# Optimization experiments

Hardware: AMD Instinct MI355X
Metric: run time of the kernel (lower is better)

Reference implementation:

```python
import jax, jax.numpy as jnp
import numpy as np

B, T = 64, 4096
K = 67            # 25 body + 21 + 21 hand keypoints
D = 256           # first_layer_size
C = 7             # num_classes
THR = 0.1         # confidence_threshold
EPS = 1e-5        # BatchNorm eps


def setup_inputs() -> dict:
    key = jax.random.key(0)
    ks = jax.random.split(key, 8)
    body = jax.random.normal(ks[0], (B, T, 75), dtype=jnp.float32)
    hand_right = jax.random.normal(ks[1], (B, T, 63), dtype=jnp.float32)
    hand_left = jax.random.normal(ks[2], (B, T, 63), dtype=jnp.float32)
    length = jax.random.randint(ks[3], (B,), 1, T + 1, dtype=jnp.int64)
    W1 = jax.random.normal(ks[4], (2 * K, D), dtype=jnp.float32) * 0.05
    b1 = jnp.zeros((D,), dtype=jnp.float32)
    gamma = jnp.ones((D,), dtype=jnp.float32)
    beta = jnp.zeros((D,), dtype=jnp.float32)
    Wc = jax.random.normal(ks[5], (D, C), dtype=jnp.float32) * 0.05
    bc = jnp.zeros((C,), dtype=jnp.float32)
    return {"body": body, "hand_right": hand_right, "hand_left": hand_left,
            "length": length, "W1": W1, "b1": b1, "gamma": gamma,
            "beta": beta, "Wc": Wc, "bc": bc}


def reference(body, hand_right, hand_left, length, W1, b1, gamma, beta, Wc, bc):
    # concat keypoint streams -> [B, T, 3K] -> [B, T, K, 3]
    feats = jnp.concatenate([body, hand_right, hand_left], axis=2)
    feats = feats.reshape(feats.shape[0], feats.shape[1], -1, 3)
    x, y, conf = feats[..., 0], feats[..., 1], feats[..., 2]
    conf = (conf > THR).astype(feats.dtype)
    # gate coords by confidence, flatten to [B, T, 2K]
    pos = jnp.stack([x * conf, y * conf], axis=3)
    pos = pos.reshape(pos.shape[0], pos.shape[1], -1)
    # static MLP: Linear + ReLU -> [B, T, D]
    sf = jax.nn.relu(jnp.einsum("btf,fd->btd", pos, W1) + b1)
    # masked max pool over valid timesteps (vectorized segment-max)
    mask = jnp.arange(sf.shape[1])[None, :] < length[:, None]      # [B, T]
    pooled = jnp.max(jnp.where(mask[:, :, None], sf, -jnp.inf), axis=1)  # [B, D]
    # BatchNorm1d (training mode: batch statistics)
    mean = pooled.mean(axis=0)
    var = pooled.var(axis=0)
    bn = (pooled - mean) / jnp.sqrt(var + EPS) * gamma + beta
    # classifier
    return bn @ Wc + bc
```

## Files before the change

### kernel.cpp

```cpp
#include <hip/hip_runtime.h>
#include <hip/hip_bf16.h>

#define B_   64
#define T_   4096
#define K_   67
#define F_   134
#define FP_  160
#define D_   256
#define C_   7
#define THR_ 0.1f
#define EPS_ 1e-5f
#define NXB_ 16

typedef __bf16 bf16x8 __attribute__((ext_vector_type(8)));
typedef float  f32x4  __attribute__((ext_vector_type(4)));

typedef __attribute__((address_space(1))) const unsigned int guint;
typedef __attribute__((address_space(3))) unsigned int luint;


__device__ __forceinline__ int get_len(const int* L, int b) {
    return (L[1] == 0) ? L[2 * b] : L[b];
}

__global__ void convert_w1(const float* __restrict__ W1, __bf16* __restrict__ W1bf) {
    __shared__ float tile[32][33];
    const int d0 = blockIdx.x * 32, f0 = blockIdx.y * 32;
    const int tx = threadIdx.x & 31, ty = threadIdx.x >> 5;
#pragma unroll
    for (int r = 0; r < 32; r += 8) {
        int f = f0 + ty + r;
        tile[ty + r][tx] = (f < F_) ? W1[f * D_ + d0 + tx] : 0.f;
    }
    __syncthreads();
#pragma unroll
    for (int r = 0; r < 32; r += 8) {
        int d = d0 + ty + r;
        W1bf[d * FP_ + f0 + tx] = (__bf16)tile[tx][ty + r];
    }
}

__global__ __launch_bounds__(256, 2)
void fused_mlp_pool(const float* __restrict__ body,
                    const float* __restrict__ hr,
                    const float* __restrict__ hl,
                    const int*   __restrict__ length,
                    const float* __restrict__ b1,
                    const __bf16* __restrict__ W1bf,
                    float* __restrict__ pooled)
{
    const int b   = blockIdx.y;
    const int len = get_len(length, b);
    const int nt  = (len + 31) >> 5;
    if ((int)blockIdx.x >= nt) return;

    __shared__ __align__(16) float  raw[2][6432];
    __shared__ __align__(16) __bf16 As[10 * 512];

    const int tid  = threadIdx.x;
    const int wave = tid >> 6;
    const int lane = tid & 63;
    const int quad = lane >> 4;
    const int l16  = lane & 15;
    const int dbase = wave * 64;

    const long rowb = (long)b * T_;

    auto stage = [&](int jt, int bufi) {
        const float* bodyt = body + (rowb + (long)jt * 32) * 75;
        const float* hrt   = hr   + (rowb + (long)jt * 32) * 63;
        const float* hlt   = hl   + (rowb + (long)jt * 32) * 63;
        char* rw = (char*)raw[bufi];
        for (int i = wave; i < 10; i += 4) {
            int off = i * 256 + lane * 4;
            if (off < 2400)
                __builtin_amdgcn_global_load_lds((guint*)(bodyt + off),
                                                 (luint*)(rw + off * 4), 16, 0, 0);
        }
        for (int i = wave; i < 8; i += 4) {
            int off = i * 256 + lane * 4;
            if (off < 2016) {
                __builtin_amdgcn_global_load_lds((guint*)(hrt + off),
                                                 (luint*)(rw + 9600 + off * 4), 16, 0, 0);
                __builtin_amdgcn_global_load_lds((guint*)(hlt + off),
                                                 (luint*)(rw + 17664 + off * 4), 16, 0, 0);
            }
        }
    };

    stage(blockIdx.x, 0);

    bf16x8 bfrag[4][5];
    float  b1v[4];
#pragma unroll
    for (int n = 0; n < 4; n++) {
        int d = dbase + n * 16 + l16;
        const __bf16* p = W1bf + d * FP_ + quad * 8;
#pragma unroll
        for (int kt = 0; kt < 5; kt++)
            bfrag[n][kt] = *(const bf16x8*)(p + kt * 32);
        b1v[n] = b1[d];
    }

    int roffv[8], wv[8];
    {
        const int t  = ((tid >> 5) & 3) * 8 + ((tid >> 2) & 7);
        const int kb = ((tid >> 7) & 1) * 4 + (tid & 3);
#pragma unroll
        for (int it = 0; it < 8; it++) {
            int k = it * 8 + kb;
            roffv[it] = (k < 25) ? t * 75 + 3 * k
                       : (k < 46) ? 2400 + t * 63 + 3 * (k - 25)
                                  : 4416 + t * 63 + 3 * (k - 46);
            wv[it] = ((t >> 4) * 5 + (k >> 4)) * 256
                   + (((k >> 2) & 3) * 16 + (t & 15)) * 4 + (k & 3);
        }
    }
    int roff_c = 0, w_c = 0;
    if (tid < 96) {
        int t = tid & 31, k = 64 + (tid >> 5);
        roff_c = 4416 + t * 63 + 3 * (k - 46);
        w_c = ((t >> 4) * 5 + (k >> 4)) * 256
            + (((k >> 2) & 3) * 16 + (t & 15)) * 4 + (k & 3);
    }

    for (int i = tid; i < 416; i += 256) {
        int t = i & 31, kp = 67 + (i >> 5);
        int w = ((t >> 4) * 5 + (kp >> 4)) * 256
              + (((kp >> 2) & 3) * 16 + (t & 15)) * 4 + (kp & 3);
        ((unsigned int*)As)[w] = 0u;
    }

    float runmax[4] = {0.f, 0.f, 0.f, 0.f};
    int cur = 0;

    for (int j = blockIdx.x; j < nt; j += NXB_) {
        const bool hasnext = (j + NXB_ < nt);
        if (hasnext) stage(j + NXB_, cur ^ 1);

        if (hasnext) {
            if (wave < 2) asm volatile("s_waitcnt vmcnt(7) lgkmcnt(0)\n\ts_barrier" ::: "memory");
            else          asm volatile("s_waitcnt vmcnt(6) lgkmcnt(0)\n\ts_barrier" ::: "memory");
        } else {
            asm volatile("s_waitcnt vmcnt(0) lgkmcnt(0)\n\ts_barrier" ::: "memory");
        }

        const float* rw = raw[cur];
#pragma unroll
        for (int it = 0; it < 8; it++) {
            float x = rw[roffv[it]], y = rw[roffv[it] + 1], cf = rw[roffv[it] + 2];
            bool g = cf > THR_;
            x = g ? x : 0.f;  y = g ? y : 0.f;
            unsigned short ux = __builtin_bit_cast(unsigned short, (__bf16)x);
            unsigned short uy = __builtin_bit_cast(unsigned short, (__bf16)y);
            ((unsigned int*)As)[wv[it]] = (unsigned int)ux | ((unsigned int)uy << 16);
        }
        if (tid < 96) {
            float x = rw[roff_c], y = rw[roff_c + 1], cf = rw[roff_c + 2];
            bool g = cf > THR_;
            x = g ? x : 0.f;  y = g ? y : 0.f;
            unsigned short ux = __builtin_bit_cast(unsigned short, (__bf16)x);
            unsigned short uy = __builtin_bit_cast(unsigned short, (__bf16)y);
            ((unsigned int*)As)[w_c] = (unsigned int)ux | ((unsigned int)uy << 16);
        }

        asm volatile("s_waitcnt lgkmcnt(0)\n\ts_barrier" ::: "memory");

        f32x4 acc[2][4];
#pragma unroll
        for (int m = 0; m < 2; m++)
#pragma unroll
            for (int n = 0; n < 4; n++)
                acc[m][n] = (f32x4){0.f, 0.f, 0.f, 0.f};
#pragma unroll
        for (int kt = 0; kt < 5; kt++) {
#pragma unroll
            for (int m = 0; m < 2; m++) {
                bf16x8 a = *(const bf16x8*)(As + (m * 5 + kt) * 512 + lane * 8);
#pragma unroll
                for (int n = 0; n < 4; n++)
                    acc[m][n] = __builtin_amdgcn_mfma_f32_16x16x32_bf16(a, bfrag[n][kt], acc[m][n], 0, 0, 0);
            }
        }

        const int tt0 = j * 32;
#pragma unroll
        for (int m = 0; m < 2; m++) {
            int trow0 = tt0 + m * 16 + quad * 4;
#pragma unroll
            for (int r = 0; r < 4; r++) {
                bool valid = (trow0 + r) < len;
#pragma unroll
                for (int n = 0; n < 4; n++) {
                    float v = acc[m][n][r] + b1v[n];
                    v = (v > 0.f) ? v : 0.f;
                    runmax[n] = (valid && v > runmax[n]) ? v : runmax[n];
                }
            }
        }
        cur ^= 1;
    }

#pragma unroll
    for (int n = 0; n < 4; n++) {
        float r = runmax[n];
        r = fmaxf(r, __shfl_xor(r, 16, 64));
        r = fmaxf(r, __shfl_xor(r, 32, 64));
        if (quad == n) {
            atomicMax((unsigned int*)(pooled + b * D_ + dbase + n * 16 + l16),
                      __float_as_uint(r));
        }
    }
}

__global__ void bn_classifier(const float* __restrict__ pooled,
                              const float* __restrict__ gamma,
                              const float* __restrict__ beta,
                              const float* __restrict__ Wc,
                              const float* __restrict__ bc,
                              float* __restrict__ out)
{
    __shared__ float scale_s[D_], shift_s[D_];
    const int tid = threadIdx.x;
    float s = 0.f, ss = 0.f;
#pragma unroll 8
    for (int b = 0; b < B_; b++) {
        float v = pooled[b * D_ + tid];
        s += v; ss += v * v;
    }
    float mean = s * (1.f / B_);
    float var  = ss * (1.f / B_) - mean * mean;
    var = fmaxf(var, 0.f);
    float sc = gamma[tid] * rsqrtf(var + EPS_);
    scale_s[tid] = sc;
    shift_s[tid] = beta[tid] - mean * sc;

    const int wv = tid >> 6, ln = tid & 63;
    float wcr[4][C_];
#pragma unroll
    for (int j = 0; j < 4; j++)
#pragma unroll
        for (int c = 0; c < C_; c++)
            wcr[j][c] = Wc[(ln * 4 + j) * C_ + c];
    __syncthreads();

    for (int b = wv * 16; b < wv * 16 + 16; b++) {
        float4 v = *(const float4*)(pooled + b * D_ + ln * 4);
        float q[4];
        q[0] = v.x * scale_s[ln * 4 + 0] + shift_s[ln * 4 + 0];
        q[1] = v.y * scale_s[ln * 4 + 1] + shift_s[ln * 4 + 1];
        q[2] = v.z * scale_s[ln * 4 + 2] + shift_s[ln * 4 + 2];
        q[3] = v.w * scale_s[ln * 4 + 3] + shift_s[ln * 4 + 3];
        float p[C_];
#pragma unroll
        for (int c = 0; c < C_; c++) p[c] = 0.f;
#pragma unroll
        for (int j = 0; j < 4; j++)
#pragma unroll
            for (int c = 0; c < C_; c++)
                p[c] += q[j] * wcr[j][c];
#pragma unroll
        for (int c = 0; c < C_; c++) {
#pragma unroll
            for (int off = 1; off < 64; off <<= 1)
                p[c] += __shfl_xor(p[c], off, 64);
        }
        if (ln == 0) {
#pragma unroll
            for (int c = 0; c < C_; c++)
                out[b * C_ + c] = p[c] + bc[c];
        }
    }
}

extern "C" void kernel_launch(void* const* d_in, const int* in_sizes, int n_in,
                              void* d_out, int out_size, void* d_ws, size_t ws_size,
                              hipStream_t stream) {
    const float* body   = (const float*)d_in[0];
    const float* hr     = (const float*)d_in[1];
    const float* hl     = (const float*)d_in[2];
    const int*   length = (const int*)  d_in[3];
    const float* W1     = (const float*)d_in[4];
    const float* b1     = (const float*)d_in[5];
    const float* gamma  = (const float*)d_in[6];
    const float* beta   = (const float*)d_in[7];
    const float* Wc     = (const float*)d_in[8];
    const float* bc     = (const float*)d_in[9];
    float* out = (float*)d_out;

    float*  pooled = (float*)d_ws;
    __bf16* W1bf   = (__bf16*)((char*)d_ws + 65536);

    hipMemsetAsync(d_ws, 0, 65536, stream);
    convert_w1<<<dim3(8, 5), dim3(256), 0, stream>>>(W1, W1bf);
    fused_mlp_pool<<<dim3(NXB_, B_), dim3(256), 0, stream>>>(body, hr, hl, length, b1, W1bf, pooled);
    bn_classifier<<<dim3(1), dim3(256), 0, stream>>>(pooled, gamma, beta, Wc, bc, out);
}
```

Before: 229.4 us.

## Rebalance pooling tiles across batches and deepen load/repack/MFMA pipeline

Uses a 1D grid in which each block handles up to eight 32-step tiles taken from eight rotated batch rows. Before, each block owned a single batch row, so work per block followed that row's length; the new mapping spreads valid tiles more evenly across blocks. The kernel also double-buffers the bf16 A tile, so the repack of the next tile overlaps the MFMAs of the current one, and it stages two tiles ahead. MFMA issue priority is raised during the matmul. In exchange it issues one atomicMax per tile instead of one per block, uses more LDS, and adds bitmask bookkeeping to skip empty tiles.

```diff
diff --git a/kernel.cpp b/kernel.cpp
--- a/kernel.cpp
+++ b/kernel.cpp
@@ -3,14 +3,13 @@
 
 #define B_   64
 #define T_   4096
-#define K_   67
 #define F_   134
 #define FP_  160
 #define D_   256
 #define C_   7
 #define THR_ 0.1f
 #define EPS_ 1e-5f
-#define NXB_ 16
+#define NQ_  16
 
 typedef __bf16 bf16x8 __attribute__((ext_vector_type(8)));
 typedef float  f32x4  __attribute__((ext_vector_type(4)));
@@ -18,10 +17,9 @@
 typedef __attribute__((address_space(1))) const unsigned int guint;
 typedef __attribute__((address_space(3))) unsigned int luint;
 
-
-__device__ __forceinline__ int get_len(const int* L, int b) {
-    return (L[1] == 0) ? L[2 * b] : L[b];
-}
+#define FBAR() asm volatile("s_waitcnt vmcnt(0) lgkmcnt(0)\n\ts_barrier" ::: "memory")
+#define LBAR() asm volatile("s_waitcnt lgkmcnt(0)\n\ts_barrier" ::: "memory")
+
 
 __global__ void convert_w1(const float* __restrict__ W1, __bf16* __restrict__ W1bf) {
     __shared__ float tile[32][33];
@@ -49,13 +47,9 @@
                     const __bf16* __restrict__ W1bf,
                     float* __restrict__ pooled)
 {
-    const int b   = blockIdx.y;
-    const int len = get_len(length, b);
-    const int nt  = (len + 31) >> 5;
-    if ((int)blockIdx.x >= nt) return;
-
-    __shared__ __align__(16) float  raw[2][6432];
-    __shared__ __align__(16) __bf16 As[10 * 512];
+    const int p = blockIdx.x;
+    const int q = p >> 6;
+    const int r = p & 63;
 
     const int tid  = threadIdx.x;
     const int wave = tid >> 6;
@@ -64,12 +58,32 @@
     const int l16  = lane & 15;
     const int dbase = wave * 64;
 
-    const long rowb = (long)b * T_;
-
-    auto stage = [&](int jt, int bufi) {
-        const float* bodyt = body + (rowb + (long)jt * 32) * 75;
-        const float* hrt   = hr   + (rowb + (long)jt * 32) * 63;
-        const float* hlt   = hl   + (rowb + (long)jt * 32) * 63;
+    const int L1 = length[1];
+    unsigned int mask = 0;
+    unsigned long long len01 = 0, len23 = 0;
+#pragma unroll
+    for (int i = 0; i < 8; i++) {
+        int bi = (r + i) & 63;
+        int li = (L1 == 0) ? length[2 * bi] : length[bi];
+        int ji = q + 16 * i;
+        if (ji * 32 < li) mask |= (1u << i);
+        if (i < 4) len01 |= (unsigned long long)(unsigned)li << (16 * i);
+        else       len23 |= (unsigned long long)(unsigned)li << (16 * (i - 4));
+    }
+    const int m = __popc(mask);
+    if (m == 0) return;
+
+    __shared__ __align__(16) float  raw[2][6432];
+    __shared__ __align__(16) __bf16 As2[2][5120];
+
+    const long rowstride = (long)T_;
+
+    auto stage = [&](int c, int bufi) {
+        const int  bb = (r + c) & 63;
+        const long t0 = (long)(q + 16 * c) * 32;
+        const float* bodyt = body + (bb * rowstride + t0) * 75;
+        const float* hrt   = hr   + (bb * rowstride + t0) * 63;
+        const float* hlt   = hl   + (bb * rowstride + t0) * 63;
         char* rw = (char*)raw[bufi];
         for (int i = wave; i < 10; i += 4) {
             int off = i * 256 + lane * 4;
@@ -88,17 +102,26 @@
         }
     };
 
-    stage(blockIdx.x, 0);
+    auto nth = [&](int n) -> int {
+        unsigned int t = mask;
+        for (int k = 0; k < n; k++) t &= t - 1;
+        return __ffs(t) - 1;
+    };
+
+    int cs  = nth(0);
+    int cs1 = (m > 1) ? nth(1) : -1;
+    stage(cs, 0);
+    if (m > 1) stage(cs1, 1);
 
     bf16x8 bfrag[4][5];
     float  b1v[4];
 #pragma unroll
     for (int n = 0; n < 4; n++) {
         int d = dbase + n * 16 + l16;
-        const __bf16* p = W1bf + d * FP_ + quad * 8;
+        const __bf16* wp = W1bf + d * FP_ + quad * 8;
 #pragma unroll
         for (int kt = 0; kt < 5; kt++)
-            bfrag[n][kt] = *(const bf16x8*)(p + kt * 32);
+            bfrag[n][kt] = *(const bf16x8*)(wp + kt * 32);
         b1v[n] = b1[d];
     }
 
@@ -124,92 +147,103 @@
             + (((k >> 2) & 3) * 16 + (t & 15)) * 4 + (k & 3);
     }
 
-    for (int i = tid; i < 416; i += 256) {
-        int t = i & 31, kp = 67 + (i >> 5);
+    for (int i = tid; i < 832; i += 256) {
+        int bufi = (i >= 416);
+        int ii = i - bufi * 416;
+        int t = ii & 31, kp = 67 + (ii >> 5);
         int w = ((t >> 4) * 5 + (kp >> 4)) * 256
               + (((kp >> 2) & 3) * 16 + (t & 15)) * 4 + (kp & 3);
-        ((unsigned int*)As)[w] = 0u;
-    }
-
-    float runmax[4] = {0.f, 0.f, 0.f, 0.f};
-    int cur = 0;
-
-    for (int j = blockIdx.x; j < nt; j += NXB_) {
-        const bool hasnext = (j + NXB_ < nt);
-        if (hasnext) stage(j + NXB_, cur ^ 1);
-
-        if (hasnext) {
-            if (wave < 2) asm volatile("s_waitcnt vmcnt(7) lgkmcnt(0)\n\ts_barrier" ::: "memory");
-            else          asm volatile("s_waitcnt vmcnt(6) lgkmcnt(0)\n\ts_barrier" ::: "memory");
-        } else {
-            asm volatile("s_waitcnt vmcnt(0) lgkmcnt(0)\n\ts_barrier" ::: "memory");
-        }
-
-        const float* rw = raw[cur];
+        ((unsigned int*)As2[bufi])[w] = 0u;
+    }
+
+    auto repack = [&](int bufi) {
+        const float* rw = raw[bufi];
+        __bf16* A = As2[bufi];
 #pragma unroll
         for (int it = 0; it < 8; it++) {
             float x = rw[roffv[it]], y = rw[roffv[it] + 1], cf = rw[roffv[it] + 2];
             bool g = cf > THR_;
-            x = g ? x : 0.f;  y = g ? y : 0.f;
-            unsigned short ux = __builtin_bit_cast(unsigned short, (__bf16)x);
-            unsigned short uy = __builtin_bit_cast(unsigned short, (__bf16)y);
-            ((unsigned int*)As)[wv[it]] = (unsigned int)ux | ((unsigned int)uy << 16);
+            unsigned short ux = __builtin_bit_cast(unsigned short, (__bf16)(g ? x : 0.f));
+            unsigned short uy = __builtin_bit_cast(unsigned short, (__bf16)(g ? y : 0.f));
+            ((unsigned int*)A)[wv[it]] = (unsigned int)ux | ((unsigned int)uy << 16);
         }
         if (tid < 96) {
             float x = rw[roff_c], y = rw[roff_c + 1], cf = rw[roff_c + 2];
             bool g = cf > THR_;
-            x = g ? x : 0.f;  y = g ? y : 0.f;
-            unsigned short ux = __builtin_bit_cast(unsigned short, (__bf16)x);
-            unsigned short uy = __builtin_bit_cast(unsigned short, (__bf16)y);
-            ((unsigned int*)As)[w_c] = (unsigned int)ux | ((unsigned int)uy << 16);
-        }
-
-        asm volatile("s_waitcnt lgkmcnt(0)\n\ts_barrier" ::: "memory");
-
+            unsigned short ux = __builtin_bit_cast(unsigned short, (__bf16)(g ? x : 0.f));
+            unsigned short uy = __builtin_bit_cast(unsigned short, (__bf16)(g ? y : 0.f));
+            ((unsigned int*)A)[w_c] = (unsigned int)ux | ((unsigned int)uy << 16);
+        }
+    };
+
+    FBAR();
+    repack(0);
+    LBAR();
+
+    for (int s = 0; s < m; s++) {
+        const int  bufc = s & 1;
+        const bool hn   = (s + 1 < m);
+        const bool hn2  = (s + 2 < m);
+        int cs2 = -1;
+        if (hn2) {
+            cs2 = cs1 + 1 + (__ffs(mask >> (cs1 + 1)) - 1);
+            stage(cs2, bufc);
+        }
+
+        if (hn) repack(bufc ^ 1);
+
+        __builtin_amdgcn_s_setprio(1);
         f32x4 acc[2][4];
 #pragma unroll
-        for (int m = 0; m < 2; m++)
+        for (int mm = 0; mm < 2; mm++)
 #pragma unroll
             for (int n = 0; n < 4; n++)
-                acc[m][n] = (f32x4){0.f, 0.f, 0.f, 0.f};
+                acc[mm][n] = (f32x4){0.f, 0.f, 0.f, 0.f};
 #pragma unroll
         for (int kt = 0; kt < 5; kt++) {
 #pragma unroll
-            for (int m = 0; m < 2; m++) {
-                bf16x8 a = *(const bf16x8*)(As + (m * 5 + kt) * 512 + lane * 8);
+            for (int mm = 0; mm < 2; mm++) {
+                bf16x8 a = *(const bf16x8*)(As2[bufc] + (mm * 5 + kt) * 512 + lane * 8);
 #pragma unroll
                 for (int n = 0; n < 4; n++)
-                    acc[m][n] = __builtin_amdgcn_mfma_f32_16x16x32_bf16(a, bfrag[n][kt], acc[m][n], 0, 0, 0);
+                    acc[mm][n] = __builtin_amdgcn_mfma_f32_16x16x32_bf16(a, bfrag[n][kt], acc[mm][n], 0, 0, 0);
             }
         }
-
-        const int tt0 = j * 32;
-#pragma unroll
-        for (int m = 0; m < 2; m++) {
-            int trow0 = tt0 + m * 16 + quad * 4;
-#pragma unroll
-            for (int r = 0; r < 4; r++) {
-                bool valid = (trow0 + r) < len;
+        __builtin_amdgcn_s_setprio(0);
+
+        const int bb   = (r + cs) & 63;
+        const int lenb = (int)((cs < 4 ? (len01 >> (cs * 16))
+                                       : (len23 >> ((cs - 4) * 16))) & 0xFFFFull);
+        const int tt0  = (q + 16 * cs) * 32;
+        float rmax[4] = {0.f, 0.f, 0.f, 0.f};
+#pragma unroll
+        for (int mm = 0; mm < 2; mm++) {
+            int trow0 = tt0 + mm * 16 + quad * 4;
+#pragma unroll
+            for (int rr = 0; rr < 4; rr++) {
+                bool valid = (trow0 + rr) < lenb;
 #pragma unroll
                 for (int n = 0; n < 4; n++) {
-                    float v = acc[m][n][r] + b1v[n];
+                    float v = acc[mm][n][rr] + b1v[n];
                     v = (v > 0.f) ? v : 0.f;
-                    runmax[n] = (valid && v > runmax[n]) ? v : runmax[n];
+                    rmax[n] = (valid && v > rmax[n]) ? v : rmax[n];
                 }
             }
         }
-        cur ^= 1;
-    }
-
-#pragma unroll
-    for (int n = 0; n < 4; n++) {
-        float r = runmax[n];
-        r = fmaxf(r, __shfl_xor(r, 16, 64));
-        r = fmaxf(r, __shfl_xor(r, 32, 64));
-        if (quad == n) {
-            atomicMax((unsigned int*)(pooled + b * D_ + dbase + n * 16 + l16),
-                      __float_as_uint(r));
-        }
+#pragma unroll
+        for (int n = 0; n < 4; n++) {
+            rmax[n] = fmaxf(rmax[n], __shfl_xor(rmax[n], 16, 64));
+            rmax[n] = fmaxf(rmax[n], __shfl_xor(rmax[n], 32, 64));
+        }
+        float rsel = (quad == 0) ? rmax[0] : (quad == 1) ? rmax[1]
+                   : (quad == 2) ? rmax[2] : rmax[3];
+
+        if (hn) FBAR();
+
+        atomicMax((unsigned int*)(pooled + bb * D_ + tid),
+                  __float_as_uint(rsel));
+
+        cs = cs1; cs1 = cs2;
     }
 }
 
@@ -293,6 +327,6 @@
 
     hipMemsetAsync(d_ws, 0, 65536, stream);
     convert_w1<<<dim3(8, 5), dim3(256), 0, stream>>>(W1, W1bf);
-    fused_mlp_pool<<<dim3(NXB_, B_), dim3(256), 0, stream>>>(body, hr, hl, length, b1, W1bf, pooled);
+    fused_mlp_pool<<<dim3(NQ_ * 64), dim3(256), 0, stream>>>(body, hr, hl, length, b1, W1bf, pooled);
     bn_classifier<<<dim3(1), dim3(256), 0, stream>>>(pooled, gamma, beta, Wc, bc, out);
 }
```

Result: no change. 233.0 us (+1.6%).
